# Kernel tuning notes

Hardware: AMD Instinct MI355X
Metric: run time of the kernel (lower is better)

## Reference

```python
import jax, jax.numpy as jnp
import numpy as np

B, S, DIM, H, DH = 2, 2048, 1024, 16, 64
EPS = 1e-6


def rms_norm(x, w):
    # x: (..., DH); computed in fp32 like the torch module
    norm = jax.lax.rsqrt(jnp.mean(jnp.square(x), axis=-1, keepdims=True) + EPS)
    return (x * norm) * w


def apply_rope(x, freqs):
    # x: (B, H, S, D), freqs: (S, D); torch code slices cos/sin to first half
    d = x.shape[-1] // 2
    cos = jnp.cos(freqs)[None, None, :, :d]
    sin = jnp.sin(freqs)[None, None, :, :d]
    x1, x2 = x[..., :d], x[..., d:]
    return jnp.concatenate([x1 * cos - x2 * sin, x2 * cos + x1 * sin], axis=-1)


def setup_inputs() -> dict:
    key = jax.random.key(0)
    ks = jax.random.split(key, 4)
    x = jax.random.normal(ks[0], (B, S, DIM), dtype=jnp.float32)
    # causal additive mask
    causal = jnp.tril(jnp.ones((S, S), dtype=bool))
    mask = jnp.where(causal, 0.0, -1e9).astype(jnp.float32)[None, None]
    # standard rope frequencies: pos * inv_freq over head_dim
    inv_freq = 1.0 / (10000.0 ** (jnp.arange(0, DH, dtype=jnp.float32) / DH))
    rope_freqs = jnp.arange(S, dtype=jnp.float32)[:, None] * inv_freq[None, :]
    total = H * DH
    w_qkv = jax.random.normal(ks[1], (3 * total, DIM), dtype=jnp.float32) * (DIM ** -0.5)
    w_out = jax.random.normal(ks[2], (DIM, total), dtype=jnp.float32) * (total ** -0.5)
    q_norm_w = jnp.ones((DH,), dtype=jnp.float32)
    k_norm_w = jnp.ones((DH,), dtype=jnp.float32)
    return {"x": x, "mask": mask, "rope_freqs": rope_freqs, "w_qkv": w_qkv,
            "w_out": w_out, "q_norm_w": q_norm_w, "k_norm_w": k_norm_w}


def reference(x, mask, rope_freqs, w_qkv, w_out, q_norm_w, k_norm_w):
    b, s, _ = x.shape
    qkv = (x @ w_qkv.T).reshape(b, s, 3, H, DH)
    q, k, v = qkv[:, :, 0], qkv[:, :, 1], qkv[:, :, 2]
    q = jnp.transpose(rms_norm(q, q_norm_w), (0, 2, 1, 3))  # (B,H,S,DH)
    k = jnp.transpose(rms_norm(k, k_norm_w), (0, 2, 1, 3))
    v = jnp.transpose(v, (0, 2, 1, 3))
    q = apply_rope(q, rope_freqs)
    k = apply_rope(k, rope_freqs)
    scale = DH ** -0.5
    attn = jnp.einsum('bhsd,bhtd->bhst', q, k) * scale + mask
    attn = jax.nn.softmax(attn, axis=-1)
    out = jnp.einsum('bhst,bhtd->bhsd', attn, v)
    out = jnp.transpose(out, (0, 2, 1, 3)).reshape(b, s, H * DH)
    return out @ w_out.T
```

## Files before the change

### kernel.cpp

```cpp
#include <hip/hip_runtime.h>
#include <hip/hip_bf16.h>
#include <stdint.h>

typedef short bf16x8 __attribute__((ext_vector_type(8)));
typedef float f32x4  __attribute__((ext_vector_type(4)));

#define MFMA_BF16(a,b,c) __builtin_amdgcn_mfma_f32_16x16x32_bf16((a),(b),(c),0,0,0)

__device__ __forceinline__ void async_ld16(const void* g, void* l) {
  __builtin_amdgcn_global_load_lds(
      (const __attribute__((address_space(1))) void*)g,
      (__attribute__((address_space(3))) void*)l, 16, 0, 0);
}

__device__ __forceinline__ unsigned short bf16_bits(float x) {
  __hip_bfloat16 h = __float2bfloat16(x);
  return *(unsigned short*)&h;
}

#define NX_C    (2 * 2048 * 1024)
#define NWQKV_C (3072 * 1024)
#define NWOUT_C (1024 * 1024)

__global__ void __launch_bounds__(256)
cvt_all(const float* __restrict__ x, const float* __restrict__ wqkv,
        const float* __restrict__ wout, __hip_bfloat16* __restrict__ dst)
{
  const int i = (blockIdx.x * 256 + threadIdx.x) * 4;
  const float* src;
  int off;
  if (i < NX_C)                { src = x;    off = i; }
  else if (i < NX_C + NWQKV_C) { src = wqkv; off = i - NX_C; }
  else                         { src = wout; off = i - NX_C - NWQKV_C; }
  const float4 v = *(const float4*)(src + off);
  ushort4 u;
  u.x = bf16_bits(v.x); u.y = bf16_bits(v.y);
  u.z = bf16_bits(v.z); u.w = bf16_bits(v.w);
  *(ushort4*)((unsigned short*)dst + i) = u;
}

template<int EPI>
__global__ void __launch_bounds__(256)
gemm_bt(const __hip_bfloat16* __restrict__ A,
        const __hip_bfloat16* __restrict__ B,
        int K,
        __hip_bfloat16* __restrict__ o0,
        __hip_bfloat16* __restrict__ o1,
        __hip_bfloat16* __restrict__ o2,
        float* __restrict__ of)
{
  __shared__ __align__(16) __hip_bfloat16 As[128 * 32];
  __shared__ __align__(16) __hip_bfloat16 Bs[128 * 32];

  const int tid  = threadIdx.x;
  const int w    = tid >> 6;
  const int lane = tid & 63;
  const int quad = lane >> 4;
  const int l15  = lane & 15;

  const int m0 = blockIdx.y * 128;
  const int n0 = blockIdx.x * 128;

  const int srow = w * 16 + (lane >> 2);
  const int skc  = (lane & 3) * 8;

  const __hip_bfloat16* Ag0 = A + (size_t)(m0 + srow)      * K + skc;
  const __hip_bfloat16* Ag1 = A + (size_t)(m0 + 64 + srow) * K + skc;
  const __hip_bfloat16* Bg0 = B + (size_t)(n0 + srow)      * K + skc;
  const __hip_bfloat16* Bg1 = B + (size_t)(n0 + 64 + srow) * K + skc;

  __hip_bfloat16* asd0 = As + w * 512;
  __hip_bfloat16* asd1 = As + 2048 + w * 512;
  __hip_bfloat16* bsd0 = Bs + w * 512;
  __hip_bfloat16* bsd1 = Bs + 2048 + w * 512;

  const int wm = (w >> 1) * 64;
  const int wn = (w & 1) * 64;

  f32x4 acc[4][4] = {};

  for (int k0 = 0; k0 < K; k0 += 32) {
    __syncthreads();
    async_ld16(Ag0 + k0, asd0);
    async_ld16(Ag1 + k0, asd1);
    async_ld16(Bg0 + k0, bsd0);
    async_ld16(Bg1 + k0, bsd1);
    __syncthreads();

    bf16x8 af[4], bfr[4];
#pragma unroll
    for (int t = 0; t < 4; ++t) {
      af[t]  = *(const bf16x8*)(As + (wm + t * 16 + l15) * 32 + quad * 8);
      bfr[t] = *(const bf16x8*)(Bs + (wn + t * 16 + l15) * 32 + quad * 8);
    }
#pragma unroll
    for (int mt = 0; mt < 4; ++mt)
#pragma unroll
      for (int nt = 0; nt < 4; ++nt)
        acc[mt][nt] = MFMA_BF16(af[mt], bfr[nt], acc[mt][nt]);
  }

  const int ldc = (int)gridDim.x * 128;
#pragma unroll
  for (int mt = 0; mt < 4; ++mt) {
#pragma unroll
    for (int nt = 0; nt < 4; ++nt) {
#pragma unroll
      for (int r = 0; r < 4; ++r) {
        const int m = m0 + wm + mt * 16 + quad * 4 + r;
        const int n = n0 + wn + nt * 16 + l15;
        if (EPI == 0) {
          const __hip_bfloat16 hv = __float2bfloat16(acc[mt][nt][r]);
          const int b = m >> 11, s = m & 2047;
          const int which = n >> 10, rem = n & 1023;
          const int h = rem >> 6, d = rem & 63;
          const int bh = b * 16 + h;
          if (which == 0)      o0[((size_t)(bh * 2048 + s) << 6) + d] = hv;
          else if (which == 1) o1[((size_t)(bh * 2048 + s) << 6) + d] = hv;
          else                 o2[((size_t)(bh * 64 + d) << 11) + s] = hv;
        } else {
          of[(size_t)m * ldc + n] = acc[mt][nt][r];
        }
      }
    }
  }
}

__global__ void __launch_bounds__(256)
norm_rope(__hip_bfloat16* __restrict__ qb,
          __hip_bfloat16* __restrict__ kb,
          const float* __restrict__ freqs,
          const float* __restrict__ qw,
          const float* __restrict__ kw)
{
  const int wid  = blockIdx.x * 4 + (threadIdx.x >> 6);
  const int lane = threadIdx.x & 63;
  const int which = wid >> 16;
  const int idx   = wid & 65535;
  const int s     = idx & 2047;

  __hip_bfloat16* buf = which ? kb : qb;
  const float* wgt = which ? kw : qw;

  const size_t base = (size_t)idx * 64;
  float x = __bfloat162float(buf[base + lane]);
  float ss = x * x;
#pragma unroll
  for (int off = 1; off < 64; off <<= 1) ss += __shfl_xor(ss, off);
  const float scale = rsqrtf(ss * (1.0f / 64.0f) + 1e-6f);
  const float y = x * scale * wgt[lane];

  const float f = freqs[s * 64 + (lane & 31)];
  const float c = cosf(f), sn = sinf(f);
  const float part = __shfl_xor(y, 32);
  float o = (lane < 32) ? (y * c - part * sn) : (y * c + part * sn);
  if (which == 0) o *= 0.125f;
  buf[base + lane] = __float2bfloat16(o);
}

__global__ void __launch_bounds__(256, 2)
attn(const __hip_bfloat16* __restrict__ q,
     const __hip_bfloat16* __restrict__ k,
     const __hip_bfloat16* __restrict__ vt,
     __hip_bfloat16* __restrict__ ao)
{
  __shared__ __align__(16) __hip_bfloat16 Ks[2][64 * 64];
  __shared__ __align__(16) __hip_bfloat16 Vs[2][64 * 64];

  const int tid  = threadIdx.x;
  const int w    = tid >> 6;
  const int lane = tid & 63;
  const int quad = lane >> 4;
  const int l15  = lane & 15;

  const int lin  = blockIdx.x;
  const int c8   = lin & 7;
  const int rest = lin >> 3;
  const int pj   = rest & 15;
  const int bh   = ((rest >> 4) << 3) + c8;
  const int b    = bh >> 4, h = bh & 15;

  const __hip_bfloat16* qb = q  + (size_t)bh * 2048 * 64;
  const __hip_bfloat16* kb = k  + (size_t)bh * 2048 * 64;
  const __hip_bfloat16* vb = vt + (size_t)bh * 64 * 2048;

  const int pr = ((l15 >> 2) * 8) + (l15 & 3);

  const int pgk  = (quad ^ (l15 & 3) ^ (((l15 >> 2) & 1) << 2)) * 8;
  const int pgk4 = pgk ^ 32;
  const int pgv  = (quad ^ (l15 & 7)) * 8;
  const int pgv4 = pgv ^ 32;

  const int sj  = lane >> 3;
  const int sp  = lane & 7;
  const int kgA = (sp ^ (sj & 3)) * 8;
  const int kgB = kgA ^ 32;
  const int vgs = (sp ^ sj) * 8;
  const int ck0 = w * 2, ck1 = w * 2 + 1;

#define STAGE(KEY0, BUF) do {                                                     \
    __hip_bfloat16* ks_ = &Ks[BUF][0];                                            \
    __hip_bfloat16* vs_ = &Vs[BUF][0];                                            \
    async_ld16(kb + (size_t)((KEY0) + ck0 * 8 + sj) * 64 + kgA, ks_ + ck0 * 512); \
    async_ld16(kb + (size_t)((KEY0) + ck1 * 8 + sj) * 64 + kgB, ks_ + ck1 * 512); \
    async_ld16(vb + (size_t)(ck0 * 8 + sj) * 2048 + (KEY0) + vgs, vs_ + ck0 * 512); \
    async_ld16(vb + (size_t)(ck1 * 8 + sj) * 2048 + (KEY0) + vgs, vs_ + ck1 * 512); \
  } while (0)

  for (int pass = 0; pass < 2; ++pass) {
    const int J  = pass ? (31 - pj) : pj;
    const int q0 = J * 64 + w * 16;
    const int qi = q0 + l15;

    const bf16x8 bq0 = *(const bf16x8*)(qb + (size_t)qi * 64 + quad * 8);
    const bf16x8 bq1 = *(const bf16x8*)(qb + (size_t)qi * 64 + 32 + quad * 8);

    f32x4 o[4] = {};
    float lsum = 0.f;

    const int ntile = J + 1;

    __syncthreads();
    STAGE(0, 0);

    for (int kt = 0; kt < ntile; ++kt) {
      const int cur = kt & 1;
      const int t0 = kt * 64;

      __syncthreads();
      if (kt + 1 < ntile) STAGE(t0 + 64, cur ^ 1);

      const __hip_bfloat16* Kc = &Ks[cur][0];
      const __hip_bfloat16* Vc = &Vs[cur][0];

      bf16x8 ka00, ka01, ka10, ka11, kb00, kb01, kb10, kb11;
      ka00 = *(const bf16x8*)(Kc + (pr)      * 64 + pgk);
      ka01 = *(const bf16x8*)(Kc + (pr)      * 64 + pgk4);
      ka10 = *(const bf16x8*)(Kc + (pr + 4)  * 64 + pgk);
      ka11 = *(const bf16x8*)(Kc + (pr + 4)  * 64 + pgk4);
      kb00 = *(const bf16x8*)(Kc + (32 + pr)     * 64 + pgk);
      kb01 = *(const bf16x8*)(Kc + (32 + pr)     * 64 + pgk4);
      kb10 = *(const bf16x8*)(Kc + (32 + pr + 4) * 64 + pgk);
      kb11 = *(const bf16x8*)(Kc + (32 + pr + 4) * 64 + pgk4);

      bf16x8 va[2][4];
#pragma unroll
      for (int dt = 0; dt < 4; ++dt) {
        va[0][dt] = *(const bf16x8*)(Vc + (dt * 16 + l15) * 64 + pgv);
        va[1][dt] = *(const bf16x8*)(Vc + (dt * 16 + l15) * 64 + pgv4);
      }

      f32x4 c00 = {}, c01 = {}, c10 = {}, c11 = {};
      c00 = MFMA_BF16(ka00, bq0, c00); c00 = MFMA_BF16(ka01, bq1, c00);
      c01 = MFMA_BF16(ka10, bq0, c01); c01 = MFMA_BF16(ka11, bq1, c01);
      c10 = MFMA_BF16(kb00, bq0, c10); c10 = MFMA_BF16(kb01, bq1, c10);
      c11 = MFMA_BF16(kb10, bq0, c11); c11 = MFMA_BF16(kb11, bq1, c11);

      float e00[4], e01[4], e10[4], e11[4];
#pragma unroll
      for (int r = 0; r < 4; ++r) {
        e00[r] = c00[r]; e01[r] = c01[r]; e10[r] = c10[r]; e11[r] = c11[r];
      }

      if (kt == ntile - 1) {
#pragma unroll
        for (int r = 0; r < 4; ++r) {
          const int k0v = t0 + 8 * quad + r;
          if (k0v      > qi) e00[r] = -1e30f;
          if (k0v + 4  > qi) e01[r] = -1e30f;
          if (k0v + 32 > qi) e10[r] = -1e30f;
          if (k0v + 36 > qi) e11[r] = -1e30f;
        }
      }

      float rs = 0.f;
#pragma unroll
      for (int r = 0; r < 4; ++r) {
        e00[r] = __expf(e00[r] - 8.0f);
        e01[r] = __expf(e01[r] - 8.0f);
        e10[r] = __expf(e10[r] - 8.0f);
        e11[r] = __expf(e11[r] - 8.0f);
        rs += (e00[r] + e01[r]) + (e10[r] + e11[r]);
      }
      lsum += rs;

      bf16x8 pf0, pf1;
#pragma unroll
      for (int r = 0; r < 4; ++r) {
        pf0[r] = (short)bf16_bits(e00[r]);  pf0[r + 4] = (short)bf16_bits(e01[r]);
        pf1[r] = (short)bf16_bits(e10[r]);  pf1[r + 4] = (short)bf16_bits(e11[r]);
      }

#pragma unroll
      for (int dt = 0; dt < 4; ++dt) {
        o[dt] = MFMA_BF16(va[0][dt], pf0, o[dt]);
        o[dt] = MFMA_BF16(va[1][dt], pf1, o[dt]);
      }
    }

    lsum += __shfl_xor(lsum, 16);
    lsum += __shfl_xor(lsum, 32);

    const float inv = 1.0f / lsum;
    const size_t row = ((size_t)(b * 2048 + qi)) * 1024 + h * 64;
#pragma unroll
    for (int dt = 0; dt < 4; ++dt) {
      ushort4 u;
      u.x = bf16_bits(o[dt][0] * inv);
      u.y = bf16_bits(o[dt][1] * inv);
      u.z = bf16_bits(o[dt][2] * inv);
      u.w = bf16_bits(o[dt][3] * inv);
      *(ushort4*)((unsigned short*)ao + row + dt * 16 + quad * 4) = u;
    }
  }
#undef STAGE
}

extern "C" void kernel_launch(void* const* d_in, const int* in_sizes, int n_in,
                              void* d_out, int out_size, void* d_ws, size_t ws_size,
                              hipStream_t stream)
{
  const float* x    = (const float*)d_in[0];
  const float* rf   = (const float*)d_in[2];
  const float* wqkv = (const float*)d_in[3];
  const float* wout = (const float*)d_in[4];
  const float* qw   = (const float*)d_in[5];
  const float* kw   = (const float*)d_in[6];

  const size_t NE = (size_t)2 * 16 * 2048 * 64;

  __hip_bfloat16* qb  = (__hip_bfloat16*)d_ws;
  __hip_bfloat16* kb  = qb  + NE;
  __hip_bfloat16* vt  = kb  + NE;
  __hip_bfloat16* ao  = vt  + NE;
  __hip_bfloat16* xb  = ao  + NE;
  __hip_bfloat16* wqb = xb  + NX_C;
  __hip_bfloat16* wob = wqb + NWQKV_C;

  cvt_all<<<(NX_C + NWQKV_C + NWOUT_C) / 1024, 256, 0, stream>>>(x, wqkv, wout, xb);

  gemm_bt<0><<<dim3(24, 32), 256, 0, stream>>>(xb, wqb, 1024, qb, kb, vt, nullptr);
  norm_rope<<<32768, 256, 0, stream>>>(qb, kb, rf, qw, kw);
  attn<<<512, 256, 0, stream>>>(qb, kb, vt, ao);
  gemm_bt<1><<<dim3(8, 32), 256, 0, stream>>>(ao, wob, 1024,
                                              nullptr, nullptr, nullptr, (float*)d_out);
}
```

Before: 226.5 us.

## Double GEMM K-tile to 64 with XOR-swizzled LDS layout

The GEMM kernel now stages a 128x64 K-slice of A and B per iteration instead of 128x32, halving the number of barrier pairs per K loop. The LDS layout uses an XOR swizzle on the 16-byte column groups so that the wider rows do not cause bank conflicts on the MFMA fragment reads. LDS usage per block doubles, which may reduce occupancy, and the loop is still not double-buffered.

```diff
diff --git a/kernel.cpp b/kernel.cpp
--- a/kernel.cpp
+++ b/kernel.cpp
@@ -49,8 +49,8 @@
         __hip_bfloat16* __restrict__ o2,
         float* __restrict__ of)
 {
-  __shared__ __align__(16) __hip_bfloat16 As[128 * 32];
-  __shared__ __align__(16) __hip_bfloat16 Bs[128 * 32];
+  __shared__ __align__(16) __hip_bfloat16 As[128 * 64];
+  __shared__ __align__(16) __hip_bfloat16 Bs[128 * 64];
 
   const int tid  = threadIdx.x;
   const int w    = tid >> 6;
@@ -61,37 +61,42 @@
   const int m0 = blockIdx.y * 128;
   const int n0 = blockIdx.x * 128;
 
-  const int srow = w * 16 + (lane >> 2);
-  const int skc  = (lane & 3) * 8;
-
-  const __hip_bfloat16* Ag0 = A + (size_t)(m0 + srow)      * K + skc;
-  const __hip_bfloat16* Ag1 = A + (size_t)(m0 + 64 + srow) * K + skc;
-  const __hip_bfloat16* Bg0 = B + (size_t)(n0 + srow)      * K + skc;
-  const __hip_bfloat16* Bg1 = B + (size_t)(n0 + 64 + srow) * K + skc;
-
-  __hip_bfloat16* asd0 = As + w * 512;
-  __hip_bfloat16* asd1 = As + 2048 + w * 512;
-  __hip_bfloat16* bsd0 = Bs + w * 512;
-  __hip_bfloat16* bsd1 = Bs + 2048 + w * 512;
+  const int sj = lane >> 3;
+  const int sg = ((lane & 7) ^ sj) * 8;
+
+  const int pg0 = (((quad ^ (l15 & 3)) | (((l15 >> 2) & 1) << 2))) * 8;
+  const int pg1 = pg0 ^ 32;
 
   const int wm = (w >> 1) * 64;
   const int wn = (w & 1) * 64;
 
   f32x4 acc[4][4] = {};
 
-  for (int k0 = 0; k0 < K; k0 += 32) {
+  for (int k0 = 0; k0 < K; k0 += 64) {
     __syncthreads();
-    async_ld16(Ag0 + k0, asd0);
-    async_ld16(Ag1 + k0, asd1);
-    async_ld16(Bg0 + k0, bsd0);
-    async_ld16(Bg1 + k0, bsd1);
+#pragma unroll
+    for (int j = 0; j < 4; ++j) {
+      const int c = w * 4 + j;
+      async_ld16(A + (size_t)(m0 + c * 8 + sj) * K + k0 + sg, As + c * 512);
+      async_ld16(B + (size_t)(n0 + c * 8 + sj) * K + k0 + sg, Bs + c * 512);
+    }
     __syncthreads();
 
     bf16x8 af[4], bfr[4];
 #pragma unroll
     for (int t = 0; t < 4; ++t) {
-      af[t]  = *(const bf16x8*)(As + (wm + t * 16 + l15) * 32 + quad * 8);
-      bfr[t] = *(const bf16x8*)(Bs + (wn + t * 16 + l15) * 32 + quad * 8);
+      af[t]  = *(const bf16x8*)(As + (wm + t * 16 + l15) * 64 + pg0);
+      bfr[t] = *(const bf16x8*)(Bs + (wn + t * 16 + l15) * 64 + pg0);
+    }
+#pragma unroll
+    for (int mt = 0; mt < 4; ++mt)
+#pragma unroll
+      for (int nt = 0; nt < 4; ++nt)
+        acc[mt][nt] = MFMA_BF16(af[mt], bfr[nt], acc[mt][nt]);
+#pragma unroll
+    for (int t = 0; t < 4; ++t) {
+      af[t]  = *(const bf16x8*)(As + (wm + t * 16 + l15) * 64 + pg1);
+      bfr[t] = *(const bf16x8*)(Bs + (wn + t * 16 + l15) * 64 + pg1);
     }
 #pragma unroll
     for (int mt = 0; mt < 4; ++mt)
```

After: 216.4 us. -4.5%, faster.
